# Performance work log

Hardware: AMD Instinct MI355X
Metric: run time of the kernel (lower is better)

Reference implementation:

```python
import jax, jax.numpy as jnp
import numpy as np

B, N, D, H = 4, 4096, 1024, 16
HD = D // H  # 64
EPS_NORM = 1e-12  # F.normalize eps
EPS_LN = 1e-5     # layernorm eps


def setup_inputs() -> dict:
    key = jax.random.key(0)
    ks = jax.random.split(key, 9)
    s = 0.02
    return {
        "x": jax.random.normal(ks[0], (B, N, D), jnp.float32),
        "Wq": jax.random.normal(ks[1], (D, D), jnp.float32) * s,
        "Wk": jax.random.normal(ks[2], (D, D), jnp.float32) * s,
        "Wv": jax.random.normal(ks[3], (D, D), jnp.float32) * s,
        "Wf": jax.random.normal(ks[4], (H, D), jnp.float32) * s,
        "Wg1": jax.random.normal(ks[5], (HD, D), jnp.float32) * s,
        "Wg2": jax.random.normal(ks[6], (D, HD), jnp.float32) * s,
        "ln_w": jnp.ones((D,), jnp.float32),
        "Wo": jax.random.normal(ks[7], (D, D), jnp.float32) * s,
    }


def _silu(x):
    return x * jax.nn.sigmoid(x)


def _simple_gla(q, k, v, f):
    # q,k,v: [B,N,H,HD], f: [B,N,H] log-decay. Recurrence:
    #   S_t = exp(f_t) * S_{t-1} + k_t v_t^T ;  o_t = q_t^T S_t  (scale=1)
    qT = jnp.moveaxis(q, 1, 0)  # [N,B,H,HD]
    kT = jnp.moveaxis(k, 1, 0)
    vT = jnp.moveaxis(v, 1, 0)
    fT = jnp.moveaxis(f, 1, 0)  # [N,B,H]

    def step(S, inp):
        qt, kt, vt, ft = inp
        S = jnp.exp(ft)[..., None, None] * S + kt[..., :, None] * vt[..., None, :]
        o = jnp.einsum('bhk,bhkv->bhv', qt, S)
        return S, o

    S0 = jnp.zeros((q.shape[0], q.shape[2], q.shape[3], v.shape[3]), q.dtype)
    _, o = jax.lax.scan(step, S0, (qT, kT, vT, fT))
    return jnp.moveaxis(o, 0, 1)  # [B,N,H,HD]


def reference(x, Wq, Wk, Wv, Wf, Wg1, Wg2, ln_w, Wo):
    b, n, d = x.shape
    q = _silu(x @ Wq.T).reshape(b, n, H, HD)
    k = _silu(x @ Wk.T).reshape(b, n, H, HD)
    v = _silu(x @ Wv.T).reshape(b, n, H, HD)
    f = jax.nn.log_sigmoid(x @ Wf.T)  # [B,N,H] scalar per-head log decay
    # F.normalize(k, p=2, dim=-1)
    k = k / jnp.maximum(jnp.linalg.norm(k, axis=-1, keepdims=True), EPS_NORM)

    o = _simple_gla(q, k, v, f).reshape(b, n, d)

    # output gate: sigmoid(Linear(d->hd) -> Linear(hd->d))
    gate = jax.nn.sigmoid((x @ Wg1.T) @ Wg2.T)
    o = o * gate

    # layernorm without bias
    mu = jnp.mean(o, axis=-1, keepdims=True)
    xc = o - mu
    var = jnp.mean(xc * xc, axis=-1, keepdims=True)
    o = xc / jnp.sqrt(var + EPS_LN) * ln_w

    return o @ Wo.T
```

## Files before the change

kernel.cpp:

```cpp
#include <hip/hip_runtime.h>
#include <stdint.h>


#define NWIDE 3200

typedef __attribute__((ext_vector_type(4))) float f32x4;
typedef __attribute__((ext_vector_type(4))) unsigned short u16x4;
typedef __attribute__((ext_vector_type(8))) unsigned short u16x8;
typedef __attribute__((ext_vector_type(8))) __bf16 bf16x8;

__device__ __forceinline__ float bf2f(unsigned short u) {
    union { unsigned int i; float f; } c; c.i = ((unsigned int)u) << 16; return c.f;
}
__device__ __forceinline__ unsigned short f2bf(float f) {
    union { float f; unsigned int i; } c; c.f = f;
    return (unsigned short)((c.i + 0x7fffu + ((c.i >> 16) & 1u)) >> 16);
}
__device__ __forceinline__ float siluf(float x) { return x / (1.f + __expf(-x)); }
__device__ __forceinline__ float logsigf(float z) {
    return (z >= 0.f) ? -log1pf(__expf(-z)) : (z - log1pf(__expf(z)));
}
__device__ __forceinline__ f32x4 MFMA(bf16x8 a, bf16x8 b, f32x4 c) {
    return __builtin_amdgcn_mfma_f32_16x16x32_bf16(a, b, c, 0, 0, 0);
}
__device__ __forceinline__ void lds16(const void* g, void* l) {
    __builtin_amdgcn_global_load_lds(
        (const __attribute__((address_space(1))) unsigned int*)(uintptr_t)g,
        (__attribute__((address_space(3))) unsigned int*)(unsigned int)(uintptr_t)l,
        16, 0, 0);
}

__global__ __launch_bounds__(256) void k_convert(const float* __restrict__ src,
                                                 unsigned short* __restrict__ dst, int n4) {
    int i = blockIdx.x * 256 + threadIdx.x;
    if (i >= n4) return;
    f32x4 v = ((const f32x4*)src)[i];
    u16x4 o;
#pragma unroll
    for (int e = 0; e < 4; e++) o[e] = f2bf(v[e]);
    ((u16x4*)dst)[i] = o;
}

__global__ __launch_bounds__(256) void k_wcat(const float* __restrict__ Wq, const float* __restrict__ Wk,
                                              const float* __restrict__ Wv, const float* __restrict__ Wf,
                                              const float* __restrict__ Wg1, unsigned short* __restrict__ Wcat) {
    const int r = blockIdx.x, t = threadIdx.x;
    const float* src = nullptr; int sr = r;
    if (r < 1024) { src = Wq; }
    else if (r < 2048) { src = Wk; sr = r - 1024; }
    else if (r < 3072) { src = Wv; sr = r - 2048; }
    else if (r < 3088) { src = Wf; sr = r - 3072; }
    else if (r < 3152) { src = Wg1; sr = r - 3088; }
    u16x4 o;
    if (src) {
        f32x4 v = *(const f32x4*)&src[(size_t)sr * 1024 + 4 * t];
#pragma unroll
        for (int e = 0; e < 4; e++) o[e] = f2bf(v[e]);
    } else {
        o[0] = 0; o[1] = 0; o[2] = 0; o[3] = 0;
    }
    *(u16x4*)&Wcat[(size_t)r * 1024 + 4 * t] = o;
}

template <int MODE>
__global__ __launch_bounds__(256)
void k_gemm(const unsigned short* __restrict__ A, const unsigned short* __restrict__ Bw,
            void* __restrict__ outp, float* __restrict__ zbuf, int M, int N, int K, int ldOut) {
    __shared__ __align__(16) unsigned short As[128 * 64];
    __shared__ __align__(16) unsigned short Bs[128 * 64];
    const int tid = threadIdx.x;
    const int w = tid >> 6, lane = tid & 63;
    const int m0 = blockIdx.x * 128, n0 = blockIdx.y * 128;
    const int fr = lane & 15, fg = lane >> 4;
    const int wr = w >> 1, wc = w & 1;
    const int srow = lane >> 3;
    const int schunk = (lane & 7) ^ (srow & 7);
    f32x4 acc[4][4] = {};
    const int kc = K >> 6;
    for (int kt = 0; kt < kc; ++kt) {
        const int k0 = kt << 6;
        __syncthreads();
#pragma unroll
        for (int q = 0; q < 4; q++) {
            const int rr = 32 * w + 8 * q;
            lds16(A + (size_t)(m0 + rr + srow) * K + k0 + schunk * 8, &As[rr * 64]);
            lds16(Bw + (size_t)(n0 + rr + srow) * K + k0 + schunk * 8, &Bs[rr * 64]);
        }
        __syncthreads();
        bf16x8 av[4][2], bv[4][2];
#pragma unroll
        for (int i = 0; i < 4; i++)
#pragma unroll
            for (int ks = 0; ks < 2; ks++) {
                const int row = 64 * wr + 16 * i + fr;
                av[i][ks] = *(const bf16x8*)&As[row * 64 + (((ks * 4 + fg) ^ (row & 7)) << 3)];
            }
#pragma unroll
        for (int j = 0; j < 4; j++)
#pragma unroll
            for (int ks = 0; ks < 2; ks++) {
                const int row = 64 * wc + 16 * j + fr;
                bv[j][ks] = *(const bf16x8*)&Bs[row * 64 + (((ks * 4 + fg) ^ (row & 7)) << 3)];
            }
#pragma unroll
        for (int i = 0; i < 4; i++)
#pragma unroll
            for (int j = 0; j < 4; j++)
#pragma unroll
                for (int ks = 0; ks < 2; ks++)
                    acc[i][j] = MFMA(av[i][ks], bv[j][ks], acc[i][j]);
    }
    const int nb = n0 + 64 * wc;
    if (MODE == 1) {
        float* O = (float*)outp;
#pragma unroll
        for (int i = 0; i < 4; i++)
#pragma unroll
            for (int j = 0; j < 4; j++) {
                const int gc = nb + 16 * j + fr;
#pragma unroll
                for (int r = 0; r < 4; r++)
                    O[(size_t)(m0 + 64 * wr + 16 * i + 4 * fg + r) * ldOut + gc] = acc[i][j][r];
            }
        return;
    }
    unsigned short* Y = (unsigned short*)outp;
    if (nb >= 3072) {
#pragma unroll
        for (int i = 0; i < 4; i++)
#pragma unroll
            for (int j = 0; j < 4; j++) {
                const int gc = nb + 16 * j + fr;
#pragma unroll
                for (int r = 0; r < 4; r++) {
                    const int gr = m0 + 64 * wr + 16 * i + 4 * fg + r;
                    const float v = acc[i][j][r];
                    if (gc < 3088) {
                        if (gc >= 3072) zbuf[gr * 16 + (gc - 3072)] = v;
                    } else if (gc < 3152) {
                        Y[(size_t)gr * ldOut + gc] = f2bf(v);
                    }
                }
            }
    } else {
#pragma unroll
        for (int i = 0; i < 4; i++)
#pragma unroll
            for (int j = 0; j < 4; j++) {
                const int gc = nb + 16 * j + fr;
#pragma unroll
                for (int r = 0; r < 4; r++)
                    Y[(size_t)(m0 + 64 * wr + 16 * i + 4 * fg + r) * ldOut + gc] = f2bf(acc[i][j][r]);
            }
    }
}

__global__ void k_cumsum(const float* __restrict__ zbuf, float* __restrict__ cbuf) {
    const int cid = blockIdx.x, t = threadIdx.x;
    const int bh = cid >> 6, ic = cid & 63;
    const int b = bh >> 4, h = bh & 15;
    float v = logsigf(zbuf[(size_t)(b * 4096 + ic * 64 + t) * 16 + h]);
#pragma unroll
    for (int off = 1; off < 64; off <<= 1) {
        float u = __shfl_up(v, (unsigned)off, 64);
        if (t >= off) v += u;
    }
    cbuf[(size_t)cid * 64 + t] = v;
}

__global__ __launch_bounds__(256)
void k_chunk_kv(const unsigned short* __restrict__ Y, const float* __restrict__ cbuf,
                unsigned short* __restrict__ St) {
    __shared__ __align__(16) unsigned short Kt[64 * 72];
    __shared__ __align__(16) unsigned short Vt[64 * 72];
    __shared__ float cs[64];
    const int cid = blockIdx.x, tid = threadIdx.x;
    const int bh = cid >> 6, ic = cid & 63;
    const int b = bh >> 4, h = bh & 15;
    if (tid < 64) cs[tid] = cbuf[(size_t)cid * 64 + tid];
    __syncthreads();
    const int s = tid >> 2, c0 = (tid & 3) << 4;
    const float wdec = __expf(cs[63] - cs[s]);
    const size_t rowg = (size_t)(b * 4096 + ic * 64 + s) * NWIDE;
    u16x8 k0v = *(const u16x8*)&Y[rowg + 1024 + h * 64 + c0];
    u16x8 k1v = *(const u16x8*)&Y[rowg + 1024 + h * 64 + c0 + 8];
    u16x8 v0v = *(const u16x8*)&Y[rowg + 2048 + h * 64 + c0];
    u16x8 v1v = *(const u16x8*)&Y[rowg + 2048 + h * 64 + c0 + 8];
    float kf[16]; float ss = 0.f;
#pragma unroll
    for (int e = 0; e < 8; e++) { kf[e] = siluf(bf2f(k0v[e])); ss += kf[e] * kf[e]; }
#pragma unroll
    for (int e = 0; e < 8; e++) { kf[8 + e] = siluf(bf2f(k1v[e])); ss += kf[8 + e] * kf[8 + e]; }
    ss += __shfl_xor(ss, 1, 64);
    ss += __shfl_xor(ss, 2, 64);
    const float sc = wdec / fmaxf(sqrtf(ss), 1e-12f);
#pragma unroll
    for (int e = 0; e < 8; e++) {
        Kt[(c0 + e) * 72 + s] = f2bf(kf[e] * sc);
        Kt[(c0 + 8 + e) * 72 + s] = f2bf(kf[8 + e] * sc);
        Vt[(c0 + e) * 72 + s] = f2bf(siluf(bf2f(v0v[e])));
        Vt[(c0 + 8 + e) * 72 + s] = f2bf(siluf(bf2f(v1v[e])));
    }
    __syncthreads();
    const int w = tid >> 6, lane = tid & 63;
    const int fr = lane & 15, fg = lane >> 4;
    f32x4 acc[4] = {};
#pragma unroll
    for (int ks = 0; ks < 2; ks++) {
        bf16x8 a = *(const bf16x8*)&Kt[(16 * w + fr) * 72 + ks * 32 + fg * 8];
#pragma unroll
        for (int j = 0; j < 4; j++)
            acc[j] = MFMA(a, *(const bf16x8*)&Vt[(16 * j + fr) * 72 + ks * 32 + fg * 8], acc[j]);
    }
    unsigned short* outp = St + (size_t)cid * 4096;
#pragma unroll
    for (int j = 0; j < 4; j++)
#pragma unroll
        for (int r = 0; r < 4; r++)
            outp[(16 * w + 4 * fg + r) * 64 + 16 * j + fr] = f2bf(acc[j][r]);
}

__global__ void k_scan(unsigned short* __restrict__ St, const float* __restrict__ cbuf) {
    const int bh = blockIdx.x >> 4;
    const int e = ((blockIdx.x & 15) << 8) + threadIdx.x;
    float S = 0.f;
    const size_t base = (size_t)bh * 64 * 4096 + e;
    for (int i = 0; i < 64; i++) {
        const float d = __expf(cbuf[(bh * 64 + i) * 64 + 63]);
        const float m = bf2f(St[base + (size_t)i * 4096]);
        St[base + (size_t)i * 4096] = f2bf(S);
        S = d * S + m;
    }
}

__global__ __launch_bounds__(256)
void k_chunk_out(const unsigned short* __restrict__ Y, const float* __restrict__ cbuf,
                 const unsigned short* __restrict__ St, const unsigned short* __restrict__ Wg2b,
                 unsigned short* __restrict__ og) {
    __shared__ __align__(16) unsigned short Qs[64 * 72];
    __shared__ __align__(16) unsigned short Ks[64 * 72];
    __shared__ __align__(16) unsigned short Vt[64 * 72];
    __shared__ __align__(16) unsigned short S0[64 * 72];
    __shared__ __align__(16) unsigned short G1[64 * 72];
    __shared__ __align__(16) unsigned short W2[64 * 72];
    __shared__ __align__(16) unsigned short Pl[4 * 16 * 72];
    __shared__ float cs[64];
    const int cid = blockIdx.x, tid = threadIdx.x;
    const int bh = cid >> 6, ic = cid & 63;
    const int b = bh >> 4, h = bh & 15;
    if (tid < 64) cs[tid] = cbuf[(size_t)cid * 64 + tid];
    const int s = tid >> 2, c0 = (tid & 3) << 4;
    const size_t rowg = (size_t)(b * 4096 + ic * 64 + s) * NWIDE;
    {
        u16x8 q0 = *(const u16x8*)&Y[rowg + h * 64 + c0];
        u16x8 q1 = *(const u16x8*)&Y[rowg + h * 64 + c0 + 8];
        u16x8 o0, o1;
#pragma unroll
        for (int e = 0; e < 8; e++) { o0[e] = f2bf(siluf(bf2f(q0[e]))); o1[e] = f2bf(siluf(bf2f(q1[e]))); }
        *(u16x8*)&Qs[s * 72 + c0] = o0;
        *(u16x8*)&Qs[s * 72 + c0 + 8] = o1;
    }
    {
        u16x8 k0v = *(const u16x8*)&Y[rowg + 1024 + h * 64 + c0];
        u16x8 k1v = *(const u16x8*)&Y[rowg + 1024 + h * 64 + c0 + 8];
        float kf[16]; float ssn = 0.f;
#pragma unroll
        for (int e = 0; e < 8; e++) { kf[e] = siluf(bf2f(k0v[e])); ssn += kf[e] * kf[e]; }
#pragma unroll
        for (int e = 0; e < 8; e++) { kf[8 + e] = siluf(bf2f(k1v[e])); ssn += kf[8 + e] * kf[8 + e]; }
        ssn += __shfl_xor(ssn, 1, 64);
        ssn += __shfl_xor(ssn, 2, 64);
        const float scn = 1.f / fmaxf(sqrtf(ssn), 1e-12f);
        u16x8 o0, o1;
#pragma unroll
        for (int e = 0; e < 8; e++) { o0[e] = f2bf(kf[e] * scn); o1[e] = f2bf(kf[8 + e] * scn); }
        *(u16x8*)&Ks[s * 72 + c0] = o0;
        *(u16x8*)&Ks[s * 72 + c0 + 8] = o1;
    }
    *(u16x8*)&G1[s * 72 + c0] = *(const u16x8*)&Y[rowg + 3088 + c0];
    *(u16x8*)&G1[s * 72 + c0 + 8] = *(const u16x8*)&Y[rowg + 3088 + c0 + 8];
    *(u16x8*)&W2[s * 72 + c0] = *(const u16x8*)&Wg2b[(size_t)(h * 64 + s) * 64 + c0];
    *(u16x8*)&W2[s * 72 + c0 + 8] = *(const u16x8*)&Wg2b[(size_t)(h * 64 + s) * 64 + c0 + 8];
    {
        u16x8 v0v = *(const u16x8*)&Y[rowg + 2048 + h * 64 + c0];
        u16x8 v1v = *(const u16x8*)&Y[rowg + 2048 + h * 64 + c0 + 8];
        u16x8 s0v = *(const u16x8*)&St[(size_t)cid * 4096 + s * 64 + c0];
        u16x8 s1v = *(const u16x8*)&St[(size_t)cid * 4096 + s * 64 + c0 + 8];
#pragma unroll
        for (int e = 0; e < 8; e++) {
            Vt[(c0 + e) * 72 + s] = f2bf(siluf(bf2f(v0v[e])));
            Vt[(c0 + 8 + e) * 72 + s] = f2bf(siluf(bf2f(v1v[e])));
            S0[(c0 + e) * 72 + s] = s0v[e];
            S0[(c0 + 8 + e) * 72 + s] = s1v[e];
        }
    }
    __syncthreads();
    const int w = tid >> 6, lane = tid & 63;
    const int fr = lane & 15, fg = lane >> 4;
    bf16x8 aq[2];
#pragma unroll
    for (int ks = 0; ks < 2; ks++) aq[ks] = *(const bf16x8*)&Qs[(16 * w + fr) * 72 + ks * 32 + fg * 8];
    f32x4 sc[4] = {};
#pragma unroll
    for (int ks = 0; ks < 2; ks++)
#pragma unroll
        for (int j = 0; j < 4; j++)
            sc[j] = MFMA(aq[ks], *(const bf16x8*)&Ks[(16 * j + fr) * 72 + ks * 32 + fg * 8], sc[j]);
    const int tl = 16 * w + 4 * fg;
#pragma unroll
    for (int j = 0; j < 4; j++)
#pragma unroll
        for (int r = 0; r < 4; r++) {
            const int tt = tl + r, ss2 = 16 * j + fr;
            float p = (ss2 <= tt) ? sc[j][r] * __expf(cs[tt] - cs[ss2]) : 0.f;
            Pl[w * (16 * 72) + (4 * fg + r) * 72 + ss2] = f2bf(p);
        }
    __syncthreads();
    f32x4 ov[4] = {};
#pragma unroll
    for (int ks = 0; ks < 2; ks++) {
        bf16x8 ap = *(const bf16x8*)&Pl[w * (16 * 72) + fr * 72 + ks * 32 + fg * 8];
#pragma unroll
        for (int j = 0; j < 4; j++)
            ov[j] = MFMA(ap, *(const bf16x8*)&Vt[(16 * j + fr) * 72 + ks * 32 + fg * 8], ov[j]);
    }
    f32x4 qs[4] = {};
#pragma unroll
    for (int ks = 0; ks < 2; ks++)
#pragma unroll
        for (int j = 0; j < 4; j++)
            qs[j] = MFMA(aq[ks], *(const bf16x8*)&S0[(16 * j + fr) * 72 + ks * 32 + fg * 8], qs[j]);
    bf16x8 ag[2];
#pragma unroll
    for (int ks = 0; ks < 2; ks++) ag[ks] = *(const bf16x8*)&G1[(16 * w + fr) * 72 + ks * 32 + fg * 8];
    f32x4 gl[4] = {};
#pragma unroll
    for (int ks = 0; ks < 2; ks++)
#pragma unroll
        for (int j = 0; j < 4; j++)
            gl[j] = MFMA(ag[ks], *(const bf16x8*)&W2[(16 * j + fr) * 72 + ks * 32 + fg * 8], gl[j]);
#pragma unroll
    for (int j = 0; j < 4; j++)
#pragma unroll
        for (int r = 0; r < 4; r++) {
            const int tt = tl + r;
            const float o = ov[j][r] + __expf(cs[tt]) * qs[j][r];
            const float g = 1.f / (1.f + __expf(-gl[j][r]));
            og[(size_t)(b * 4096 + ic * 64 + tt) * 1024 + h * 64 + 16 * j + fr] = f2bf(o * g);
        }
}

__global__ __launch_bounds__(256)
void k_ln(unsigned short* __restrict__ og, const float* __restrict__ lnw) {
    __shared__ float red[8];
    const int r = blockIdx.x, t = threadIdx.x;
    unsigned short* p = og + (size_t)r * 1024;
    u16x4 a = *(u16x4*)&p[4 * t];
    float x[4]; float s = 0.f, ssum = 0.f;
#pragma unroll
    for (int e = 0; e < 4; e++) { x[e] = bf2f(a[e]); s += x[e]; ssum += x[e] * x[e]; }
#pragma unroll
    for (int m = 1; m < 64; m <<= 1) { s += __shfl_xor(s, m, 64); ssum += __shfl_xor(ssum, m, 64); }
    const int w = t >> 6;
    if ((t & 63) == 0) { red[w] = s; red[4 + w] = ssum; }
    __syncthreads();
    s = red[0] + red[1] + red[2] + red[3];
    ssum = red[4] + red[5] + red[6] + red[7];
    const float mu = s * (1.f / 1024.f);
    const float var = ssum * (1.f / 1024.f) - mu * mu;
    const float rs = rsqrtf(var + 1e-5f);
    u16x4 o;
#pragma unroll
    for (int e = 0; e < 4; e++) o[e] = f2bf((x[e] - mu) * rs * lnw[4 * t + e]);
    *(u16x4*)&p[4 * t] = o;
}

extern "C" void kernel_launch(void* const* d_in, const int* in_sizes, int n_in,
                              void* d_out, int out_size, void* d_ws, size_t ws_size,
                              hipStream_t stream) {
    const float* x = (const float*)d_in[0];
    const float* Wq = (const float*)d_in[1];
    const float* Wk = (const float*)d_in[2];
    const float* Wv = (const float*)d_in[3];
    const float* Wf = (const float*)d_in[4];
    const float* Wg1 = (const float*)d_in[5];
    const float* Wg2 = (const float*)d_in[6];
    const float* lnw = (const float*)d_in[7];
    const float* Wo = (const float*)d_in[8];
    char* ws = (char*)d_ws;
    unsigned short* xb = (unsigned short*)(ws + 0);
    unsigned short* Yb = (unsigned short*)(ws + 33554432LL);
    unsigned short* Wcat = (unsigned short*)(ws + 138412032LL);
    unsigned short* Wob = (unsigned short*)(ws + 144965632LL);
    unsigned short* Wg2b = (unsigned short*)(ws + 147062784LL);
    float* zbuf = (float*)(ws + 147193856LL);
    float* cbuf = (float*)(ws + 148242432LL);
    unsigned short* St = (unsigned short*)(ws + 149291008LL);
    unsigned short* og = xb;

    k_convert<<<16384, 256, 0, stream>>>(x, xb, 4194304);
    k_wcat<<<3200, 256, 0, stream>>>(Wq, Wk, Wv, Wf, Wg1, Wcat);
    k_convert<<<1024, 256, 0, stream>>>(Wo, Wob, 262144);
    k_convert<<<64, 256, 0, stream>>>(Wg2, Wg2b, 16384);
    k_gemm<0><<<dim3(128, 25), 256, 0, stream>>>(xb, Wcat, Yb, zbuf, 16384, 3200, 1024, 3200);
    k_cumsum<<<4096, 64, 0, stream>>>(zbuf, cbuf);
    k_chunk_kv<<<4096, 256, 0, stream>>>(Yb, cbuf, St);
    k_scan<<<1024, 256, 0, stream>>>(St, cbuf);
    k_chunk_out<<<4096, 256, 0, stream>>>(Yb, cbuf, St, Wg2b, og);
    k_ln<<<16384, 256, 0, stream>>>(og, lnw);
    k_gemm<1><<<dim3(128, 8), 256, 0, stream>>>(og, Wob, d_out, nullptr, 16384, 1024, 1024, 1024);
}
```

Measured before the change: 340.1 us.

## Replace GEMM with 256x256 8-wave double-buffered pipelined kernel

The old 128x128 GEMM used one LDS buffer with full syncs per k-step. It is replaced by a 256x256-tile, 512-thread kernel that double-buffers A/B tiles in 128KB LDS. Global-to-LDS loads are interleaved with MFMA phases using explicit waitcnt, barriers and setprio, and tiles are remapped across the 8 XCDs. Wcat is padded to 3328 rows so N tiles of 256 divide evenly. This wastes some compute on padding and relies on fragile hand-written wait counts.

```diff
diff --git a/kernel.cpp b/kernel.cpp
--- a/kernel.cpp
+++ b/kernel.cpp
@@ -5,6 +5,7 @@
 #define NWIDE 3200
 
 typedef __attribute__((ext_vector_type(4))) float f32x4;
+typedef __attribute__((ext_vector_type(4))) unsigned int u32x4;
 typedef __attribute__((ext_vector_type(4))) unsigned short u16x4;
 typedef __attribute__((ext_vector_type(8))) unsigned short u16x8;
 typedef __attribute__((ext_vector_type(8))) __bf16 bf16x8;
@@ -28,6 +29,11 @@
         (const __attribute__((address_space(1))) unsigned int*)(uintptr_t)g,
         (__attribute__((address_space(3))) unsigned int*)(unsigned int)(uintptr_t)l,
         16, 0, 0);
+}
+__device__ __forceinline__ bf16x8 lds_rd16(unsigned addr) {
+    u32x4 r;
+    asm volatile("ds_read_b128 %0, %1" : "=v"(r) : "v"(addr));
+    return __builtin_bit_cast(bf16x8, r);
 }
 
 __global__ __launch_bounds__(256) void k_convert(const float* __restrict__ src,
@@ -62,78 +68,134 @@
     *(u16x4*)&Wcat[(size_t)r * 1024 + 4 * t] = o;
 }
 
-template <int MODE>
-__global__ __launch_bounds__(256)
-void k_gemm(const unsigned short* __restrict__ A, const unsigned short* __restrict__ Bw,
-            void* __restrict__ outp, float* __restrict__ zbuf, int M, int N, int K, int ldOut) {
-    __shared__ __align__(16) unsigned short As[128 * 64];
-    __shared__ __align__(16) unsigned short Bs[128 * 64];
+template <int I0>
+__device__ __forceinline__ void mfma16(const bf16x8* av, const bf16x8* bv, f32x4 (&acc)[8][4]) {
+#pragma unroll
+    for (int di = 0; di < 2; di++)
+#pragma unroll
+        for (int j = 0; j < 4; j++)
+#pragma unroll
+            for (int ks = 0; ks < 2; ks++)
+                acc[I0 + di][j] = MFMA(av[di * 2 + ks], bv[j * 2 + ks], acc[I0 + di][j]);
+}
+
+template <int MODE, int NKT>
+__global__ __launch_bounds__(512, 2)
+void k_gemm8(const unsigned short* __restrict__ A, const unsigned short* __restrict__ Bw,
+             void* __restrict__ outp, float* __restrict__ zbuf, int K, int NT, int ldOut) {
+    __shared__ __align__(16) char smem[131072];
+    const unsigned lbase = (unsigned)(uintptr_t)&smem[0];
     const int tid = threadIdx.x;
     const int w = tid >> 6, lane = tid & 63;
-    const int m0 = blockIdx.x * 128, n0 = blockIdx.y * 128;
     const int fr = lane & 15, fg = lane >> 4;
-    const int wr = w >> 1, wc = w & 1;
-    const int srow = lane >> 3;
-    const int schunk = (lane & 7) ^ (srow & 7);
-    f32x4 acc[4][4] = {};
-    const int kc = K >> 6;
-    for (int kt = 0; kt < kc; ++kt) {
-        const int k0 = kt << 6;
-        __syncthreads();
-#pragma unroll
-        for (int q = 0; q < 4; q++) {
-            const int rr = 32 * w + 8 * q;
-            lds16(A + (size_t)(m0 + rr + srow) * K + k0 + schunk * 8, &As[rr * 64]);
-            lds16(Bw + (size_t)(n0 + rr + srow) * K + k0 + schunk * 8, &Bs[rr * 64]);
+    const int wr = w >> 2, wc = w & 3;
+    const int bid = blockIdx.x;
+    const int cpx = gridDim.x >> 3;
+    const int sbid = (bid & 7) * cpx + (bid >> 3);
+    const int mt = sbid / NT, nt = sbid - mt * NT;
+    const int m0 = mt << 8, n0 = nt << 8;
+
+    f32x4 acc[8][4] = {};
+    bf16x8 bv[8];
+
+    auto STAGE = [&](int tile, int half) {
+        const unsigned short* G = (half < 2) ? A : Bw;
+        const int grow0 = ((half < 2) ? m0 : n0) + ((half & 1) << 7);
+        const int dstbase = ((tile & 1) << 16) + (half << 14);
+        const int k0 = tile << 6;
+#pragma unroll
+        for (int q = 0; q < 2; q++) {
+            const int slot = (q << 9) + (w << 6) + lane;
+            const int r = slot >> 3, c = slot & 7;
+            lds16(G + (size_t)(grow0 + r) * K + k0 + ((c ^ (r & 7)) << 3),
+                  smem + dstbase + (q << 13) + (w << 10));
         }
-        __syncthreads();
-        bf16x8 av[4][2], bv[4][2];
-#pragma unroll
-        for (int i = 0; i < 4; i++)
+    };
+    auto LDB = [&](int buf) {
+#pragma unroll
+        for (int j = 0; j < 4; j++)
 #pragma unroll
             for (int ks = 0; ks < 2; ks++) {
-                const int row = 64 * wr + 16 * i + fr;
-                av[i][ks] = *(const bf16x8*)&As[row * 64 + (((ks * 4 + fg) ^ (row & 7)) << 3)];
+                const int row = (wc << 6) + (j << 4) + fr;
+                const unsigned byt = (unsigned)((buf << 16) + 32768 + (row << 7) +
+                                                ((((ks << 2) + fg) ^ (row & 7)) << 4));
+                bv[j * 2 + ks] = lds_rd16(lbase + byt);
             }
-#pragma unroll
-        for (int j = 0; j < 4; j++)
+    };
+    auto LDA = [&](int buf, int i0, bf16x8* av) {
+#pragma unroll
+        for (int di = 0; di < 2; di++)
 #pragma unroll
             for (int ks = 0; ks < 2; ks++) {
-                const int row = 64 * wc + 16 * j + fr;
-                bv[j][ks] = *(const bf16x8*)&Bs[row * 64 + (((ks * 4 + fg) ^ (row & 7)) << 3)];
+                const int row = (wr << 7) + ((i0 + di) << 4) + fr;
+                const unsigned byt = (unsigned)((buf << 16) + (row << 7) +
+                                                ((((ks << 2) + fg) ^ (row & 7)) << 4));
+                av[di * 2 + ks] = lds_rd16(lbase + byt);
             }
-#pragma unroll
-        for (int i = 0; i < 4; i++)
-#pragma unroll
-            for (int j = 0; j < 4; j++)
-#pragma unroll
-                for (int ks = 0; ks < 2; ks++)
-                    acc[i][j] = MFMA(av[i][ks], bv[j][ks], acc[i][j]);
-    }
-    const int nb = n0 + 64 * wc;
+    };
+
+#define GBAR() do { asm volatile("" ::: "memory"); __builtin_amdgcn_s_barrier(); asm volatile("" ::: "memory"); } while (0)
+
+    STAGE(0, 0); STAGE(0, 1); STAGE(0, 2); STAGE(0, 3); STAGE(1, 2); STAGE(1, 3);
+    asm volatile("s_waitcnt vmcnt(4)" ::: "memory");
+    GBAR();
+
+#define PHASE(P, STILE, SHALF, GUARD)                                          \
+    do {                                                                       \
+        const int buf_ = (2 * t + ((P) >= 4 ? 1 : 0)) & 1;                     \
+        bf16x8 av[4];                                                          \
+        if (((P) & 3) == 0) LDB(buf_);                                         \
+        LDA(buf_, 2 * ((P) & 3), av);                                          \
+        const int st_ = 2 * t + (STILE);                                       \
+        if (st_ < NKT) STAGE(st_, (SHALF));                                    \
+        if (((P) & 3) == 0) asm volatile("s_waitcnt lgkmcnt(8)" ::: "memory"); \
+        GBAR();                                                                \
+        asm volatile("s_waitcnt lgkmcnt(0)" ::: "memory");                     \
+        __builtin_amdgcn_sched_barrier(0);                                     \
+        __builtin_amdgcn_s_setprio(1);                                         \
+        mfma16<2 * ((P) & 3)>(av, bv, acc);                                    \
+        __builtin_amdgcn_s_setprio(0);                                         \
+        if (((P) & 3) == 3) asm volatile("s_waitcnt vmcnt(" #GUARD ")" ::: "memory"); \
+        GBAR();                                                                \
+    } while (0)
+
+    for (int t = 0; t < NKT / 2 - 1; t++) {
+        PHASE(0, 1, 0, 4); PHASE(1, 1, 1, 4); PHASE(2, 2, 2, 4); PHASE(3, 2, 3, 4);
+        PHASE(4, 2, 0, 4); PHASE(5, 2, 1, 4); PHASE(6, 3, 2, 4); PHASE(7, 3, 3, 4);
+    }
+    {
+        const int t = NKT / 2 - 1;
+        PHASE(0, 1, 0, 0); PHASE(1, 1, 1, 0); PHASE(2, 2, 2, 0); PHASE(3, 2, 3, 0);
+        PHASE(4, 2, 0, 0); PHASE(5, 2, 1, 0); PHASE(6, 3, 2, 0); PHASE(7, 3, 3, 0);
+    }
+#undef PHASE
+#undef GBAR
+
+    const int nb = n0 + (wc << 6);
+    const int rbase = m0 + (wr << 7) + (fg << 2);
     if (MODE == 1) {
         float* O = (float*)outp;
 #pragma unroll
-        for (int i = 0; i < 4; i++)
+        for (int i = 0; i < 8; i++)
 #pragma unroll
             for (int j = 0; j < 4; j++) {
-                const int gc = nb + 16 * j + fr;
+                const int gc = nb + (j << 4) + fr;
 #pragma unroll
                 for (int r = 0; r < 4; r++)
-                    O[(size_t)(m0 + 64 * wr + 16 * i + 4 * fg + r) * ldOut + gc] = acc[i][j][r];
+                    O[(size_t)(rbase + (i << 4) + r) * ldOut + gc] = acc[i][j][r];
             }
         return;
     }
     unsigned short* Y = (unsigned short*)outp;
     if (nb >= 3072) {
 #pragma unroll
-        for (int i = 0; i < 4; i++)
+        for (int i = 0; i < 8; i++)
 #pragma unroll
             for (int j = 0; j < 4; j++) {
-                const int gc = nb + 16 * j + fr;
+                const int gc = nb + (j << 4) + fr;
 #pragma unroll
                 for (int r = 0; r < 4; r++) {
-                    const int gr = m0 + 64 * wr + 16 * i + 4 * fg + r;
+                    const int gr = rbase + (i << 4) + r;
                     const float v = acc[i][j][r];
                     if (gc < 3088) {
                         if (gc >= 3072) zbuf[gr * 16 + (gc - 3072)] = v;
@@ -144,13 +206,13 @@
             }
     } else {
 #pragma unroll
-        for (int i = 0; i < 4; i++)
+        for (int i = 0; i < 8; i++)
 #pragma unroll
             for (int j = 0; j < 4; j++) {
-                const int gc = nb + 16 * j + fr;
+                const int gc = nb + (j << 4) + fr;
 #pragma unroll
                 for (int r = 0; r < 4; r++)
-                    Y[(size_t)(m0 + 64 * wr + 16 * i + 4 * fg + r) * ldOut + gc] = f2bf(acc[i][j][r]);
+                    Y[(size_t)(rbase + (i << 4) + r) * ldOut + gc] = f2bf(acc[i][j][r]);
             }
     }
 }
@@ -391,22 +453,22 @@
     unsigned short* xb = (unsigned short*)(ws + 0);
     unsigned short* Yb = (unsigned short*)(ws + 33554432LL);
     unsigned short* Wcat = (unsigned short*)(ws + 138412032LL);
-    unsigned short* Wob = (unsigned short*)(ws + 144965632LL);
-    unsigned short* Wg2b = (unsigned short*)(ws + 147062784LL);
-    float* zbuf = (float*)(ws + 147193856LL);
-    float* cbuf = (float*)(ws + 148242432LL);
-    unsigned short* St = (unsigned short*)(ws + 149291008LL);
+    unsigned short* Wob = (unsigned short*)(ws + 145227776LL);
+    unsigned short* Wg2b = (unsigned short*)(ws + 147324928LL);
+    float* zbuf = (float*)(ws + 147456000LL);
+    float* cbuf = (float*)(ws + 148504576LL);
+    unsigned short* St = (unsigned short*)(ws + 149553152LL);
     unsigned short* og = xb;
 
     k_convert<<<16384, 256, 0, stream>>>(x, xb, 4194304);
-    k_wcat<<<3200, 256, 0, stream>>>(Wq, Wk, Wv, Wf, Wg1, Wcat);
+    k_wcat<<<3328, 256, 0, stream>>>(Wq, Wk, Wv, Wf, Wg1, Wcat);
     k_convert<<<1024, 256, 0, stream>>>(Wo, Wob, 262144);
     k_convert<<<64, 256, 0, stream>>>(Wg2, Wg2b, 16384);
-    k_gemm<0><<<dim3(128, 25), 256, 0, stream>>>(xb, Wcat, Yb, zbuf, 16384, 3200, 1024, 3200);
+    k_gemm8<0, 16><<<832, 512, 0, stream>>>(xb, Wcat, Yb, zbuf, 1024, 13, 3200);
     k_cumsum<<<4096, 64, 0, stream>>>(zbuf, cbuf);
     k_chunk_kv<<<4096, 256, 0, stream>>>(Yb, cbuf, St);
     k_scan<<<1024, 256, 0, stream>>>(St, cbuf);
     k_chunk_out<<<4096, 256, 0, stream>>>(Yb, cbuf, St, Wg2b, og);
     k_ln<<<16384, 256, 0, stream>>>(og, lnw);
-    k_gemm<1><<<dim3(128, 8), 256, 0, stream>>>(og, Wob, d_out, nullptr, 16384, 1024, 1024, 1024);
-}
+    k_gemm8<1, 16><<<256, 512, 0, stream>>>(og, Wob, d_out, nullptr, 1024, 4, 1024);
+}
```

Measured after the change: 350.8 us. 3.2% more time.

## Fold layernorm into output GEMM epilogue and merge prep/cumsum kernels

Applied to the files above, without the earlier changes.

Merges the four conversion kernels into one prep launch that also folds ln_w into Wo and precomputes per-column sums of the folded weight. The layernorm pass now only computes per-row mean and rstd, and the output GEMM applies normalization in its epilogue as rs*(acc - mu*colsum). This removes a full read-modify-write of the 32MB bf16 activation. The cumsum kernel is also fused into chunk_kv. In exchange the GEMM now consumes unnormalized bf16 activations, which shifts rounding error and adds a risk of cancellation in the mean subtraction.

```diff
diff --git a/kernel.cpp b/kernel.cpp
--- a/kernel.cpp
+++ b/kernel.cpp
@@ -30,42 +30,68 @@
         16, 0, 0);
 }
 
-__global__ __launch_bounds__(256) void k_convert(const float* __restrict__ src,
-                                                 unsigned short* __restrict__ dst, int n4) {
-    int i = blockIdx.x * 256 + threadIdx.x;
-    if (i >= n4) return;
-    f32x4 v = ((const f32x4*)src)[i];
-    u16x4 o;
-#pragma unroll
-    for (int e = 0; e < 4; e++) o[e] = f2bf(v[e]);
-    ((u16x4*)dst)[i] = o;
-}
-
-__global__ __launch_bounds__(256) void k_wcat(const float* __restrict__ Wq, const float* __restrict__ Wk,
-                                              const float* __restrict__ Wv, const float* __restrict__ Wf,
-                                              const float* __restrict__ Wg1, unsigned short* __restrict__ Wcat) {
-    const int r = blockIdx.x, t = threadIdx.x;
-    const float* src = nullptr; int sr = r;
-    if (r < 1024) { src = Wq; }
-    else if (r < 2048) { src = Wk; sr = r - 1024; }
-    else if (r < 3072) { src = Wv; sr = r - 2048; }
-    else if (r < 3088) { src = Wf; sr = r - 3072; }
-    else if (r < 3152) { src = Wg1; sr = r - 3088; }
-    u16x4 o;
-    if (src) {
-        f32x4 v = *(const f32x4*)&src[(size_t)sr * 1024 + 4 * t];
+__global__ __launch_bounds__(256)
+void k_prep(const float* __restrict__ x, const float* __restrict__ Wq, const float* __restrict__ Wk,
+            const float* __restrict__ Wv, const float* __restrict__ Wf, const float* __restrict__ Wg1,
+            const float* __restrict__ Wg2, const float* __restrict__ lnw, const float* __restrict__ Wo,
+            unsigned short* __restrict__ xb, unsigned short* __restrict__ Wcat,
+            unsigned short* __restrict__ Wob, unsigned short* __restrict__ Wg2b,
+            float* __restrict__ scol) {
+    const int blk = blockIdx.x, t = threadIdx.x;
+    if (blk < 16384) {
+        const int i = blk * 256 + t;
+        f32x4 v = ((const f32x4*)x)[i];
+        u16x4 o;
 #pragma unroll
         for (int e = 0; e < 4; e++) o[e] = f2bf(v[e]);
+        ((u16x4*)xb)[i] = o;
+    } else if (blk < 19584) {
+        const int r = blk - 16384;
+        const float* src = nullptr; int sr = r;
+        if (r < 1024) { src = Wq; }
+        else if (r < 2048) { src = Wk; sr = r - 1024; }
+        else if (r < 3072) { src = Wv; sr = r - 2048; }
+        else if (r < 3088) { src = Wf; sr = r - 3072; }
+        else if (r < 3152) { src = Wg1; sr = r - 3088; }
+        u16x4 o;
+        if (src) {
+            f32x4 v = *(const f32x4*)&src[(size_t)sr * 1024 + 4 * t];
+#pragma unroll
+            for (int e = 0; e < 4; e++) o[e] = f2bf(v[e]);
+        } else {
+            o[0] = 0; o[1] = 0; o[2] = 0; o[3] = 0;
+        }
+        *(u16x4*)&Wcat[(size_t)r * 1024 + 4 * t] = o;
+    } else if (blk < 20608) {
+        __shared__ float red[4];
+        const int c = blk - 19584;
+        f32x4 wv = *(const f32x4*)&Wo[(size_t)c * 1024 + 4 * t];
+        f32x4 lv = *(const f32x4*)&lnw[4 * t];
+        u16x4 o; float ps = 0.f;
+#pragma unroll
+        for (int e = 0; e < 4; e++) { o[e] = f2bf(wv[e] * lv[e]); ps += bf2f(o[e]); }
+        *(u16x4*)&Wob[(size_t)c * 1024 + 4 * t] = o;
+#pragma unroll
+        for (int m = 1; m < 64; m <<= 1) ps += __shfl_xor(ps, m, 64);
+        if ((t & 63) == 0) red[t >> 6] = ps;
+        __syncthreads();
+        if (t == 0) scol[c] = red[0] + red[1] + red[2] + red[3];
     } else {
-        o[0] = 0; o[1] = 0; o[2] = 0; o[3] = 0;
-    }
-    *(u16x4*)&Wcat[(size_t)r * 1024 + 4 * t] = o;
+        const int i = (blk - 20608) * 256 + t;
+        f32x4 v = ((const f32x4*)Wg2)[i];
+        u16x4 o;
+#pragma unroll
+        for (int e = 0; e < 4; e++) o[e] = f2bf(v[e]);
+        ((u16x4*)Wg2b)[i] = o;
+    }
 }
 
 template <int MODE>
 __global__ __launch_bounds__(256)
 void k_gemm(const unsigned short* __restrict__ A, const unsigned short* __restrict__ Bw,
-            void* __restrict__ outp, float* __restrict__ zbuf, int M, int N, int K, int ldOut) {
+            void* __restrict__ outp, float* __restrict__ zbuf,
+            const float* __restrict__ stats, const float* __restrict__ scol,
+            int M, int N, int K, int ldOut) {
     __shared__ __align__(16) unsigned short As[128 * 64];
     __shared__ __align__(16) unsigned short Bs[128 * 64];
     const int tid = threadIdx.x;
@@ -113,14 +139,18 @@
     const int nb = n0 + 64 * wc;
     if (MODE == 1) {
         float* O = (float*)outp;
+        float sj[4];
+#pragma unroll
+        for (int j = 0; j < 4; j++) sj[j] = scol[nb + 16 * j + fr];
 #pragma unroll
         for (int i = 0; i < 4; i++)
 #pragma unroll
-            for (int j = 0; j < 4; j++) {
-                const int gc = nb + 16 * j + fr;
-#pragma unroll
-                for (int r = 0; r < 4; r++)
-                    O[(size_t)(m0 + 64 * wr + 16 * i + 4 * fg + r) * ldOut + gc] = acc[i][j][r];
+            for (int r = 0; r < 4; r++) {
+                const int gr = m0 + 64 * wr + 16 * i + 4 * fg + r;
+                const float mu = stats[gr * 2], rs = stats[gr * 2 + 1];
+#pragma unroll
+                for (int j = 0; j < 4; j++)
+                    O[(size_t)gr * ldOut + nb + 16 * j + fr] = rs * (acc[i][j][r] - mu * sj[j]);
             }
         return;
     }
@@ -155,29 +185,25 @@
     }
 }
 
-__global__ void k_cumsum(const float* __restrict__ zbuf, float* __restrict__ cbuf) {
-    const int cid = blockIdx.x, t = threadIdx.x;
-    const int bh = cid >> 6, ic = cid & 63;
-    const int b = bh >> 4, h = bh & 15;
-    float v = logsigf(zbuf[(size_t)(b * 4096 + ic * 64 + t) * 16 + h]);
-#pragma unroll
-    for (int off = 1; off < 64; off <<= 1) {
-        float u = __shfl_up(v, (unsigned)off, 64);
-        if (t >= off) v += u;
-    }
-    cbuf[(size_t)cid * 64 + t] = v;
-}
-
 __global__ __launch_bounds__(256)
-void k_chunk_kv(const unsigned short* __restrict__ Y, const float* __restrict__ cbuf,
-                unsigned short* __restrict__ St) {
+void k_chunk_kv(const unsigned short* __restrict__ Y, const float* __restrict__ zbuf,
+                float* __restrict__ cbuf, unsigned short* __restrict__ St) {
     __shared__ __align__(16) unsigned short Kt[64 * 72];
     __shared__ __align__(16) unsigned short Vt[64 * 72];
     __shared__ float cs[64];
     const int cid = blockIdx.x, tid = threadIdx.x;
     const int bh = cid >> 6, ic = cid & 63;
     const int b = bh >> 4, h = bh & 15;
-    if (tid < 64) cs[tid] = cbuf[(size_t)cid * 64 + tid];
+    if (tid < 64) {
+        float v = logsigf(zbuf[(size_t)(b * 4096 + ic * 64 + tid) * 16 + h]);
+#pragma unroll
+        for (int off = 1; off < 64; off <<= 1) {
+            float u = __shfl_up(v, (unsigned)off, 64);
+            if (tid >= off) v += u;
+        }
+        cs[tid] = v;
+        cbuf[(size_t)cid * 64 + tid] = v;
+    }
     __syncthreads();
     const int s = tid >> 2, c0 = (tid & 3) << 4;
     const float wdec = __expf(cs[63] - cs[s]);
@@ -351,28 +377,25 @@
 }
 
 __global__ __launch_bounds__(256)
-void k_ln(unsigned short* __restrict__ og, const float* __restrict__ lnw) {
-    __shared__ float red[8];
-    const int r = blockIdx.x, t = threadIdx.x;
-    unsigned short* p = og + (size_t)r * 1024;
-    u16x4 a = *(u16x4*)&p[4 * t];
-    float x[4]; float s = 0.f, ssum = 0.f;
-#pragma unroll
-    for (int e = 0; e < 4; e++) { x[e] = bf2f(a[e]); s += x[e]; ssum += x[e] * x[e]; }
-#pragma unroll
-    for (int m = 1; m < 64; m <<= 1) { s += __shfl_xor(s, m, 64); ssum += __shfl_xor(ssum, m, 64); }
-    const int w = t >> 6;
-    if ((t & 63) == 0) { red[w] = s; red[4 + w] = ssum; }
-    __syncthreads();
-    s = red[0] + red[1] + red[2] + red[3];
-    ssum = red[4] + red[5] + red[6] + red[7];
-    const float mu = s * (1.f / 1024.f);
-    const float var = ssum * (1.f / 1024.f) - mu * mu;
-    const float rs = rsqrtf(var + 1e-5f);
-    u16x4 o;
-#pragma unroll
-    for (int e = 0; e < 4; e++) o[e] = f2bf((x[e] - mu) * rs * lnw[4 * t + e]);
-    *(u16x4*)&p[4 * t] = o;
+void k_lnstats(const unsigned short* __restrict__ og, float* __restrict__ stats) {
+    const int row = blockIdx.x * 4 + (threadIdx.x >> 6);
+    const int lane = threadIdx.x & 63;
+    const unsigned short* p = og + (size_t)row * 1024 + lane * 16;
+    u16x8 a = *(const u16x8*)p;
+    u16x8 b2 = *(const u16x8*)(p + 8);
+    float s = 0.f, q = 0.f;
+#pragma unroll
+    for (int e = 0; e < 8; e++) { float x = bf2f(a[e]); s += x; q += x * x; }
+#pragma unroll
+    for (int e = 0; e < 8; e++) { float x = bf2f(b2[e]); s += x; q += x * x; }
+#pragma unroll
+    for (int m = 1; m < 64; m <<= 1) { s += __shfl_xor(s, m, 64); q += __shfl_xor(q, m, 64); }
+    if (lane == 0) {
+        const float mu = s * (1.f / 1024.f);
+        const float var = q * (1.f / 1024.f) - mu * mu;
+        stats[row * 2] = mu;
+        stats[row * 2 + 1] = rsqrtf(var + 1e-5f);
+    }
 }
 
 extern "C" void kernel_launch(void* const* d_in, const int* in_sizes, int n_in,
@@ -396,17 +419,18 @@
     float* zbuf = (float*)(ws + 147193856LL);
     float* cbuf = (float*)(ws + 148242432LL);
     unsigned short* St = (unsigned short*)(ws + 149291008LL);
+    float* scol = (float*)(ws + 182845440LL);
+    float* stats = (float*)(ws + 182849536LL);
     unsigned short* og = xb;
 
-    k_convert<<<16384, 256, 0, stream>>>(x, xb, 4194304);
-    k_wcat<<<3200, 256, 0, stream>>>(Wq, Wk, Wv, Wf, Wg1, Wcat);
-    k_convert<<<1024, 256, 0, stream>>>(Wo, Wob, 262144);
-    k_convert<<<64, 256, 0, stream>>>(Wg2, Wg2b, 16384);
-    k_gemm<0><<<dim3(128, 25), 256, 0, stream>>>(xb, Wcat, Yb, zbuf, 16384, 3200, 1024, 3200);
-    k_cumsum<<<4096, 64, 0, stream>>>(zbuf, cbuf);
-    k_chunk_kv<<<4096, 256, 0, stream>>>(Yb, cbuf, St);
+    k_prep<<<20672, 256, 0, stream>>>(x, Wq, Wk, Wv, Wf, Wg1, Wg2, lnw, Wo,
+                                      xb, Wcat, Wob, Wg2b, scol);
+    k_gemm<0><<<dim3(128, 25), 256, 0, stream>>>(xb, Wcat, Yb, zbuf, nullptr, nullptr,
+                                                 16384, 3200, 1024, 3200);
+    k_chunk_kv<<<4096, 256, 0, stream>>>(Yb, zbuf, cbuf, St);
     k_scan<<<1024, 256, 0, stream>>>(St, cbuf);
     k_chunk_out<<<4096, 256, 0, stream>>>(Yb, cbuf, St, Wg2b, og);
-    k_ln<<<16384, 256, 0, stream>>>(og, lnw);
-    k_gemm<1><<<dim3(128, 8), 256, 0, stream>>>(og, Wob, d_out, nullptr, 16384, 1024, 1024, 1024);
-}
+    k_lnstats<<<4096, 256, 0, stream>>>(og, stats);
+    k_gemm<1><<<dim3(128, 8), 256, 0, stream>>>(og, Wob, d_out, nullptr, stats, scol,
+                                                16384, 1024, 1024, 1024);
+}
```

Result: no change. 334.6 us (-1.6%).
